# Kernel tuning notes

Hardware: AMD Instinct MI355X
Metric: run time of the kernel (lower is better)

## Reference

```python
import jax, jax.numpy as jnp
import numpy as np

INPUT_SIZE = 128
HIDDEN_SIZE = 256


def lstm_cell(x, h, c, w_ih, w_hh, b_ih, b_hh):
    # PyTorch LSTMCell gate order: i, f, g, o
    gates = x @ w_ih.T + b_ih + h @ w_hh.T + b_hh  # [B, 4H]
    i, f, g, o = jnp.split(gates, 4, axis=-1)
    c_new = jax.nn.sigmoid(f) * c + jax.nn.sigmoid(i) * jnp.tanh(g)
    h_new = jax.nn.sigmoid(o) * jnp.tanh(c_new)
    return h_new, c_new


def setup_inputs() -> dict:
    key = jax.random.key(0)
    ks = jax.random.split(key, 7)
    P, H = INPUT_SIZE, HIDDEN_SIZE
    s_ih = 1.0 / np.sqrt(H)
    inputs = jax.random.normal(ks[0], (8, 256, 64, P), dtype=jnp.float32)
    w_ih = jax.random.uniform(ks[1], (4 * H, P), jnp.float32, -s_ih, s_ih)
    w_hh = jax.random.uniform(ks[2], (4 * H, H), jnp.float32, -s_ih, s_ih)
    b_ih = jax.random.uniform(ks[3], (4 * H,), jnp.float32, -s_ih, s_ih)
    b_hh = jax.random.uniform(ks[4], (4 * H,), jnp.float32, -s_ih, s_ih)
    s_l = 1.0 / np.sqrt(H)
    w_lin = jax.random.uniform(ks[5], (P, H), jnp.float32, -s_l, s_l)
    b_lin = jax.random.uniform(ks[6], (P,), jnp.float32, -s_l, s_l)
    return {"inputs": inputs, "w_ih": w_ih, "w_hh": w_hh, "b_ih": b_ih,
            "b_hh": b_hh, "w_lin": w_lin, "b_lin": b_lin, "horizon": 32}


def reference(inputs, w_ih, w_hh, b_ih, b_hh, w_lin, b_lin, horizon):
    T, S, F, P = inputs.shape
    H = w_hh.shape[1]
    B = T * S  # tasks share weights, states are independent -> fuse batch
    x = inputs.reshape(B, F, P)
    h0 = jnp.zeros((B, H), inputs.dtype)
    c0 = jnp.zeros((B, H), inputs.dtype)

    def enc_step(carry, xt):
        h, c = carry
        h, c = lstm_cell(xt, h, c, w_ih, w_hh, b_ih, b_hh)
        return (h, c), None

    (h, c), _ = jax.lax.scan(enc_step, (h0, c0), jnp.swapaxes(x, 0, 1))
    pred = h @ w_lin.T + b_lin  # [B, P]

    def ar_step(carry, _):
        h, c, p = carry
        h, c = lstm_cell(p, h, c, w_ih, w_hh, b_ih, b_hh)
        p = h @ w_lin.T + b_lin
        return (h, c, p), p

    _, preds = jax.lax.scan(ar_step, (h, c, pred), None, length=horizon - 1)
    outs = jnp.concatenate([pred[None], preds], axis=0)  # [horizon, B, P]
    return jnp.moveaxis(outs, 0, 1).reshape(T, S, horizon, P)
```

## Files before the change

### kernel.cpp

```cpp
#include <hip/hip_runtime.h>
#include <cstdint>
#include <cstddef>

typedef short short8_t __attribute__((ext_vector_type(8)));
typedef float float4_t __attribute__((ext_vector_type(4)));

#define NRG 32

__device__ __align__(16) unsigned short g_W[1024 * 384];
__device__ __align__(16) unsigned short g_Weff[1024 * 256];
__device__ __align__(16) unsigned short g_Wlin[128 * 256];
__device__ float g_bias[1024];
__device__ float g_beff[1024];
__device__ float g_blin[128];
__device__ __align__(16) unsigned short g_hx[NRG][2][64][256];
__device__ int g_flag[NRG][4][8];

__device__ __forceinline__ unsigned short f2bf_rn(float f) {
    union { float f; unsigned int u; } v; v.f = f;
    unsigned int u = v.u;
    return (unsigned short)((u + 0x7FFFu + ((u >> 16) & 1u)) >> 16);
}
__device__ __forceinline__ float sigm(float x) { return 1.0f / (1.0f + __expf(-x)); }
__device__ __forceinline__ float tanh_fast(float x) { return 2.0f / (1.0f + __expf(-2.0f * x)) - 1.0f; }

__global__ void prep_kernel(const float* __restrict__ w_ih, const float* __restrict__ w_hh,
                            const float* __restrict__ b_ih, const float* __restrict__ b_hh,
                            const float* __restrict__ w_lin, const float* __restrict__ b_lin) {
    int idx = blockIdx.x * blockDim.x + threadIdx.x;
    int stride = gridDim.x * blockDim.x;
    for (int i = idx; i < 49152; i += stride) {
        int f = i >> 6, l = i & 63;
        int kt = f % 12, rest = f / 12;
        int s = rest & 3, wvv = (rest >> 2) & 3, g = rest >> 4;
        int n = g * 256 + wvv * 64 + s * 16 + (l & 15);
        int k0 = kt * 32 + (l >> 4) * 8;
        unsigned short* dst = g_W + f * 512 + l * 8;
#pragma unroll
        for (int j = 0; j < 8; ++j) {
            int k = k0 + j;
            float v = (k < 128) ? w_ih[n * 128 + k] : w_hh[n * 256 + (k - 128)];
            dst[j] = f2bf_rn(v);
        }
    }
    for (int i = idx; i < 4096; i += stride) {
        int f = i >> 6, l = i & 63;
        int kt = f & 7, wss = f >> 3;
        int s = wss & 1, wvv = wss >> 1;
        int n = wvv * 32 + s * 16 + (l & 15);
        int k0 = kt * 32 + (l >> 4) * 8;
        unsigned short* dst = g_Wlin + f * 512 + l * 8;
#pragma unroll
        for (int j = 0; j < 8; ++j)
            dst[j] = f2bf_rn(w_lin[n * 256 + k0 + j]);
    }
    for (int i = idx; i < 1024; i += stride) g_bias[i] = b_ih[i] + b_hh[i];
    for (int i = idx; i < 128; i += stride) g_blin[i] = b_lin[i];
    for (int i = idx; i < NRG * 32; i += stride) ((int*)g_flag)[i] = 0;
}

__global__ void prep2_kernel(const float* __restrict__ w_ih, const float* __restrict__ w_hh,
                             const float* __restrict__ w_lin, const float* __restrict__ b_ih,
                             const float* __restrict__ b_hh, const float* __restrict__ b_lin) {
    int i = blockIdx.x * 256 + threadIdx.x;
    {
        int e = i & 511, f = i >> 9;
        int l = e >> 3, j = e & 7;
        int kt2 = f & 7, rest = f >> 3;
        int s = rest & 3, w = (rest >> 2) & 3, g = rest >> 4;
        int n = g * 256 + w * 64 + s * 16 + (l & 15);
        int k = kt2 * 32 + (l >> 4) * 8 + j;
        float acc = w_hh[n * 256 + k];
#pragma unroll 4
        for (int p = 0; p < 128; ++p)
            acc += w_ih[n * 128 + p] * w_lin[p * 256 + k];
        g_Weff[f * 512 + e] = f2bf_rn(acc);
    }
    if (i < 1024) {
        float acc = b_ih[i] + b_hh[i];
        for (int p = 0; p < 128; ++p)
            acc += w_ih[i * 128 + p] * b_lin[p];
        g_beff[i] = acc;
    }
}

__global__ void __launch_bounds__(256, 1) lstm_persist(const float* __restrict__ inp,
                                                       float* __restrict__ out) {
    __shared__ __align__(16) unsigned short gw[96 * 512];
    __shared__ __align__(16) unsigned short wl_sh[8 * 512];
    __shared__ __align__(16) unsigned short tb[4][512];

    const int tid = threadIdx.x;
    const int wv = tid >> 6, l = tid & 63, l15 = l & 15, lg = l >> 4;
    const int c = blockIdx.x >> 5, rg = blockIdx.x & 31;

    for (int i = tid; i < 96 * 64; i += 256) {
        int lf = i >> 6, ch = i & 63;
        int kt = lf % 12, gs = lf / 12;
        int s2 = gs & 1, g = gs >> 1;
        int gf = ((g * 4 + (c >> 1)) * 4 + 2 * (c & 1) + s2) * 12 + kt;
        *(uint4*)&gw[lf * 512 + ch * 8] = *(const uint4*)&g_W[gf * 512 + ch * 8];
    }
    for (int i = tid; i < 8 * 64; i += 256) {
        int lf = i >> 6, ch = i & 63;
        *(uint4*)&wl_sh[lf * 512 + ch * 8] = *(const uint4*)&g_Wlin[(c * 8 + lf) * 512 + ch * 8];
    }
    float biasr[4][2], beffr[4][2];
#pragma unroll
    for (int g = 0; g < 4; ++g)
#pragma unroll
        for (int s2 = 0; s2 < 2; ++s2) {
            biasr[g][s2] = g_bias[g * 256 + c * 32 + s2 * 16 + l15];
            beffr[g][s2] = g_beff[g * 256 + c * 32 + s2 * 16 + l15];
        }
    const float blin_r = g_blin[c * 16 + l15];
    __syncthreads();

    short8_t ha[8], xa[4];
    short8_t zz = {0, 0, 0, 0, 0, 0, 0, 0};
#pragma unroll
    for (int i = 0; i < 8; ++i) ha[i] = zz;
#pragma unroll
    for (int i = 0; i < 4; ++i) xa[i] = zz;
    float c_st[2][4];
#pragma unroll
    for (int s2 = 0; s2 < 2; ++s2)
#pragma unroll
        for (int r = 0; r < 4; ++r) c_st[s2][r] = 0.0f;

    const float* xrow = inp + (size_t)(rg * 64 + wv * 16 + l15) * 8192 + lg * 8;
    float4_t xf[8];
#pragma unroll
    for (int kt = 0; kt < 4; ++kt) {
        xf[2 * kt]     = *(const float4_t*)(xrow + kt * 32);
        xf[2 * kt + 1] = *(const float4_t*)(xrow + kt * 32 + 4);
    }

    for (int t = 0; t <= 95; ++t) {
        if (t == 64) {
            __syncthreads();
            for (int i = tid; i < 64 * 64; i += 256) {
                int lf = i >> 6, ch = i & 63;
                int kt2 = lf & 7, gs = lf >> 3;
                int s2 = gs & 1, g = gs >> 1;
                int gf = ((g * 4 + (c >> 1)) * 4 + 2 * (c & 1) + s2) * 8 + kt2;
                *(uint4*)&gw[lf * 512 + ch * 8] = *(const uint4*)&g_Weff[gf * 512 + ch * 8];
            }
            __syncthreads();
        }

        float4_t acc[4][2];
        if (t < 95) {
#pragma unroll
            for (int g = 0; g < 4; ++g)
#pragma unroll
                for (int s2 = 0; s2 < 2; ++s2) {
                    float b = (t < 64) ? biasr[g][s2] : beffr[g][s2];
                    acc[g][s2] = (float4_t){b, b, b, b};
                }
        }

        if (t < 64) {
#pragma unroll
            for (int kt = 0; kt < 4; ++kt) {
                short8_t vv;
                vv[0] = (short)f2bf_rn(xf[2 * kt][0]); vv[1] = (short)f2bf_rn(xf[2 * kt][1]);
                vv[2] = (short)f2bf_rn(xf[2 * kt][2]); vv[3] = (short)f2bf_rn(xf[2 * kt][3]);
                vv[4] = (short)f2bf_rn(xf[2 * kt + 1][0]); vv[5] = (short)f2bf_rn(xf[2 * kt + 1][1]);
                vv[6] = (short)f2bf_rn(xf[2 * kt + 1][2]); vv[7] = (short)f2bf_rn(xf[2 * kt + 1][3]);
                xa[kt] = vv;
            }
            if (t <= 62) {
                const float* xp = xrow + (t + 1) * 128;
#pragma unroll
                for (int kt = 0; kt < 4; ++kt) {
                    xf[2 * kt]     = *(const float4_t*)(xp + kt * 32);
                    xf[2 * kt + 1] = *(const float4_t*)(xp + kt * 32 + 4);
                }
            }
#pragma unroll
            for (int kt = 0; kt < 4; ++kt)
#pragma unroll
                for (int g = 0; g < 4; ++g)
#pragma unroll
                    for (int s2 = 0; s2 < 2; ++s2) {
                        const short8_t wf = *(const short8_t*)&gw[((g * 2 + s2) * 12 + kt) * 512 + l * 8];
                        acc[g][s2] = __builtin_amdgcn_mfma_f32_16x16x32_bf16(xa[kt], wf, acc[g][s2], 0, 0, 0);
                    }
        }

        if (t > 0) {
            __builtin_amdgcn_sched_barrier(0);
            const int* fp = &g_flag[rg][wv][l & 7];
            int fv, guard = 0;
            do {
                asm volatile("global_load_dword %0, %1, off sc0 sc1\n\ts_waitcnt vmcnt(0)"
                             : "=v"(fv) : "v"(fp) : "memory");
            } while (!__all(fv >= t) && ++guard < (1 << 15));
            __builtin_amdgcn_sched_barrier(0);
            const char* hb = (const char*)&g_hx[rg][(t - 1) & 1][wv * 16 + l15][lg * 8];
#pragma unroll
            for (int kt = 0; kt < 8; ++kt)
                asm volatile("global_load_dwordx4 %0, %1, off sc0 sc1"
                             : "=v"(ha[kt]) : "v"(hb + kt * 64) : "memory");
            asm volatile("s_waitcnt vmcnt(0)" ::: "memory");
            __builtin_amdgcn_sched_barrier(0);
        }

        if (t < 95) {
            if (t > 0) {
                if (t < 64) {
#pragma unroll
                    for (int kt = 4; kt < 12; ++kt)
#pragma unroll
                        for (int g = 0; g < 4; ++g)
#pragma unroll
                            for (int s2 = 0; s2 < 2; ++s2) {
                                const short8_t wf = *(const short8_t*)&gw[((g * 2 + s2) * 12 + kt) * 512 + l * 8];
                                acc[g][s2] = __builtin_amdgcn_mfma_f32_16x16x32_bf16(ha[kt - 4], wf, acc[g][s2], 0, 0, 0);
                            }
                } else {
#pragma unroll
                    for (int kt = 0; kt < 8; ++kt)
#pragma unroll
                        for (int g = 0; g < 4; ++g)
#pragma unroll
                            for (int s2 = 0; s2 < 2; ++s2) {
                                const short8_t wf = *(const short8_t*)&gw[((g * 2 + s2) * 8 + kt) * 512 + l * 8];
                                acc[g][s2] = __builtin_amdgcn_mfma_f32_16x16x32_bf16(ha[kt], wf, acc[g][s2], 0, 0, 0);
                            }
                }
            }
            char* tbw = (char*)&tb[wv][0];
#pragma unroll
            for (int s2 = 0; s2 < 2; ++s2)
#pragma unroll
                for (int r = 0; r < 4; ++r) {
                    float ip = acc[0][s2][r], fpv = acc[1][s2][r];
                    float gp = acc[2][s2][r], op = acc[3][s2][r];
                    float cn = sigm(fpv) * c_st[s2][r] + sigm(ip) * tanh_fast(gp);
                    c_st[s2][r] = cn;
                    float hv = sigm(op) * tanh_fast(cn);
                    int m = lg * 4 + r;
                    int boff = (m * 64 + (s2 * 16 + l15) * 2) ^ (lg << 4);
                    *(unsigned short*)(tbw + boff) = f2bf_rn(hv);
                }
            int roff = (l15 * 64 + (lg << 4)) ^ ((l15 >> 2) << 4);
            short8_t hv8 = *(const short8_t*)(tbw + roff);
            char* dst = (char*)&g_hx[rg][t & 1][wv * 16 + l15][c * 32 + lg * 8];
            asm volatile("global_store_dwordx4 %0, %1, off sc0 sc1" :: "v"(dst), "v"(hv8) : "memory");
            asm volatile("s_waitcnt vmcnt(0)" ::: "memory");
            if (l == 0) {
                int* fw = &g_flag[rg][wv][c];
                int nv = t + 1;
                asm volatile("global_store_dword %0, %1, off sc0 sc1" :: "v"(fw), "v"(nv) : "memory");
            }
        }

        if (t >= 64) {
            float4_t pacc = {blin_r, blin_r, blin_r, blin_r};
#pragma unroll
            for (int kt = 0; kt < 8; ++kt) {
                const short8_t wf = *(const short8_t*)&wl_sh[kt * 512 + l * 8];
                pacc = __builtin_amdgcn_mfma_f32_16x16x32_bf16(ha[kt], wf, pacc, 0, 0, 0);
            }
            int ko = t - 64;
            float* orow = out + ((size_t)(rg * 64 + wv * 16 + lg * 4) * 32 + ko) * 128 + c * 16 + l15;
#pragma unroll
            for (int r = 0; r < 4; ++r)
                orow[(size_t)r * 32 * 128] = pacc[r];
        }
    }
}

extern "C" void kernel_launch(void* const* d_in, const int* in_sizes, int n_in,
                              void* d_out, int out_size, void* d_ws, size_t ws_size,
                              hipStream_t stream) {
    const float* inp   = (const float*)d_in[0];
    const float* w_ih  = (const float*)d_in[1];
    const float* w_hh  = (const float*)d_in[2];
    const float* b_ih  = (const float*)d_in[3];
    const float* b_hh  = (const float*)d_in[4];
    const float* w_lin = (const float*)d_in[5];
    const float* b_lin = (const float*)d_in[6];
    (void)in_sizes; (void)n_in; (void)d_ws; (void)ws_size; (void)out_size;

    prep_kernel<<<128, 256, 0, stream>>>(w_ih, w_hh, b_ih, b_hh, w_lin, b_lin);
    prep2_kernel<<<1024, 256, 0, stream>>>(w_ih, w_hh, w_lin, b_ih, b_hh, b_lin);
    lstm_persist<<<256, 256, 0, stream>>>(inp, (float*)d_out);
}
```

Baseline: 606.2 us.

## Interleave two row groups per block to hide cross-block sync latency

Each persistent block now handles two independent row groups (A and B) and alternates between them. While one group's compute runs, the flag poll and the hidden-state loads for the other group are already in flight, which is meant to hide the global-memory handoff between blocks on the recurrence. The grid is halved to 128 blocks, so half as many CUs are in use and each block does twice the MFMA work per step. The spin guard limit is also raised.

```diff
diff --git a/kernel.cpp b/kernel.cpp
--- a/kernel.cpp
+++ b/kernel.cpp
@@ -84,6 +84,124 @@
     }
 }
 
+#define WAITCNT0 do { asm volatile("s_waitcnt vmcnt(0)" ::: "memory"); \
+                      __builtin_amdgcn_sched_barrier(0); } while (0)
+
+#define POLL(RG, WANT) do { \
+    __builtin_amdgcn_sched_barrier(0); \
+    const int* fp_ = &g_flag[RG][wv][l & 7]; \
+    int fv_, guard_ = 0; \
+    do { \
+        asm volatile("global_load_dword %0, %1, off sc0 sc1\n\ts_waitcnt vmcnt(0)" \
+                     : "=v"(fv_) : "v"(fp_) : "memory"); \
+    } while (!__all(fv_ >= (WANT)) && ++guard_ < (1 << 18)); \
+    __builtin_amdgcn_sched_barrier(0); \
+} while (0)
+
+#define ISSUE_HA(HA, RG, PAR) do { \
+    const char* hb_ = (const char*)&g_hx[RG][PAR][wv * 16 + l15][lg * 8]; \
+    _Pragma("unroll") \
+    for (int kt_ = 0; kt_ < 8; ++kt_) \
+        asm volatile("global_load_dwordx4 %0, %1, off sc0 sc1" \
+                     : "=v"(HA[kt_]) : "v"(hb_ + kt_ * 64) : "memory"); \
+} while (0)
+
+#define ISSUE_XF(XF, XROW, TT) do { \
+    const char* xp_ = (const char*)((XROW) + (size_t)(TT) * 128); \
+    _Pragma("unroll") \
+    for (int q_ = 0; q_ < 8; ++q_) \
+        asm volatile("global_load_dwordx4 %0, %1, off" \
+                     : "=v"(XF[q_]) : "v"(xp_ + ((q_ >> 1) * 128 + (q_ & 1) * 16)) : "memory"); \
+} while (0)
+
+#define CONVERT_XA(XF) do { \
+    _Pragma("unroll") \
+    for (int kt_ = 0; kt_ < 4; ++kt_) { \
+        short8_t vv_; \
+        vv_[0] = (short)f2bf_rn(XF[2*kt_][0]); vv_[1] = (short)f2bf_rn(XF[2*kt_][1]); \
+        vv_[2] = (short)f2bf_rn(XF[2*kt_][2]); vv_[3] = (short)f2bf_rn(XF[2*kt_][3]); \
+        vv_[4] = (short)f2bf_rn(XF[2*kt_+1][0]); vv_[5] = (short)f2bf_rn(XF[2*kt_+1][1]); \
+        vv_[6] = (short)f2bf_rn(XF[2*kt_+1][2]); vv_[7] = (short)f2bf_rn(XF[2*kt_+1][3]); \
+        xa[kt_] = vv_; \
+    } \
+} while (0)
+
+#define XPART() do { \
+    _Pragma("unroll") \
+    for (int kt_ = 0; kt_ < 4; ++kt_) \
+        _Pragma("unroll") \
+        for (int g_ = 0; g_ < 4; ++g_) \
+            _Pragma("unroll") \
+            for (int s2_ = 0; s2_ < 2; ++s2_) { \
+                const short8_t wf_ = *(const short8_t*)&gw[((g_*2+s2_)*12+kt_)*512 + l*8]; \
+                acc[g_][s2_] = __builtin_amdgcn_mfma_f32_16x16x32_bf16(xa[kt_], wf_, acc[g_][s2_], 0, 0, 0); \
+            } \
+} while (0)
+
+#define HPART_ENC(HA) do { \
+    _Pragma("unroll") \
+    for (int kt_ = 4; kt_ < 12; ++kt_) \
+        _Pragma("unroll") \
+        for (int g_ = 0; g_ < 4; ++g_) \
+            _Pragma("unroll") \
+            for (int s2_ = 0; s2_ < 2; ++s2_) { \
+                const short8_t wf_ = *(const short8_t*)&gw[((g_*2+s2_)*12+kt_)*512 + l*8]; \
+                acc[g_][s2_] = __builtin_amdgcn_mfma_f32_16x16x32_bf16(HA[kt_-4], wf_, acc[g_][s2_], 0, 0, 0); \
+            } \
+} while (0)
+
+#define HPART_AR(HA) do { \
+    _Pragma("unroll") \
+    for (int kt_ = 0; kt_ < 8; ++kt_) \
+        _Pragma("unroll") \
+        for (int g_ = 0; g_ < 4; ++g_) \
+            _Pragma("unroll") \
+            for (int s2_ = 0; s2_ < 2; ++s2_) { \
+                const short8_t wf_ = *(const short8_t*)&gw[((g_*2+s2_)*8+kt_)*512 + l*8]; \
+                acc[g_][s2_] = __builtin_amdgcn_mfma_f32_16x16x32_bf16(HA[kt_], wf_, acc[g_][s2_], 0, 0, 0); \
+            } \
+} while (0)
+
+#define POINTWISE_STORE(RG, CST, PAR, FLAGVAL) do { \
+    char* tbw_ = (char*)&tb[wv][0]; \
+    _Pragma("unroll") \
+    for (int s2_ = 0; s2_ < 2; ++s2_) \
+        _Pragma("unroll") \
+        for (int r_ = 0; r_ < 4; ++r_) { \
+            float ip_ = acc[0][s2_][r_], fp2_ = acc[1][s2_][r_]; \
+            float gp_ = acc[2][s2_][r_], op_ = acc[3][s2_][r_]; \
+            float cn_ = sigm(fp2_) * CST[s2_][r_] + sigm(ip_) * tanh_fast(gp_); \
+            CST[s2_][r_] = cn_; \
+            float hv_ = sigm(op_) * tanh_fast(cn_); \
+            int m_ = lg * 4 + r_; \
+            int boff_ = (m_ * 64 + (s2_ * 16 + l15) * 2) ^ (lg << 4); \
+            *(unsigned short*)(tbw_ + boff_) = f2bf_rn(hv_); \
+        } \
+    int roff_ = (l15 * 64 + (lg << 4)) ^ ((l15 >> 2) << 4); \
+    short8_t hv8_ = *(const short8_t*)(tbw_ + roff_); \
+    char* dst_ = (char*)&g_hx[RG][PAR][wv * 16 + l15][c * 32 + lg * 8]; \
+    asm volatile("global_store_dwordx4 %0, %1, off sc0 sc1" :: "v"(dst_), "v"(hv8_) : "memory"); \
+    WAITCNT0; \
+    if (l == 0) { \
+        int* fw_ = &g_flag[RG][wv][c]; \
+        int nv_ = (FLAGVAL); \
+        asm volatile("global_store_dword %0, %1, off sc0 sc1" :: "v"(fw_), "v"(nv_) : "memory"); \
+    } \
+} while (0)
+
+#define PRED(HA, RG, KO) do { \
+    float4_t pacc_ = {blin_r, blin_r, blin_r, blin_r}; \
+    _Pragma("unroll") \
+    for (int kt_ = 0; kt_ < 8; ++kt_) { \
+        const short8_t wf_ = *(const short8_t*)&wl_sh[kt_ * 512 + l * 8]; \
+        pacc_ = __builtin_amdgcn_mfma_f32_16x16x32_bf16(HA[kt_], wf_, pacc_, 0, 0, 0); \
+    } \
+    float* orow_ = out + ((size_t)((RG) * 64 + wv * 16 + lg * 4) * 32 + (KO)) * 128 + c * 16 + l15; \
+    _Pragma("unroll") \
+    for (int r_ = 0; r_ < 4; ++r_) \
+        orow_[(size_t)r_ * 32 * 128] = pacc_[r_]; \
+} while (0)
+
 __global__ void __launch_bounds__(256, 1) lstm_persist(const float* __restrict__ inp,
                                                        float* __restrict__ out) {
     __shared__ __align__(16) unsigned short gw[96 * 512];
@@ -92,7 +210,8 @@
 
     const int tid = threadIdx.x;
     const int wv = tid >> 6, l = tid & 63, l15 = l & 15, lg = l >> 4;
-    const int c = blockIdx.x >> 5, rg = blockIdx.x & 31;
+    const int c = blockIdx.x >> 4, srg = blockIdx.x & 15;
+    const int rgA = 2 * srg, rgB = 2 * srg + 1;
 
     for (int i = tid; i < 96 * 64; i += 256) {
         int lf = i >> 6, ch = i & 63;
@@ -116,25 +235,18 @@
     const float blin_r = g_blin[c * 16 + l15];
     __syncthreads();
 
-    short8_t ha[8], xa[4];
-    short8_t zz = {0, 0, 0, 0, 0, 0, 0, 0};
-#pragma unroll
-    for (int i = 0; i < 8; ++i) ha[i] = zz;
-#pragma unroll
-    for (int i = 0; i < 4; ++i) xa[i] = zz;
-    float c_st[2][4];
+    short8_t haA[8], haB[8], xa[4];
+    float4_t xfA[8], xfB[8];
+    float cA[2][4], cB[2][4];
 #pragma unroll
     for (int s2 = 0; s2 < 2; ++s2)
 #pragma unroll
-        for (int r = 0; r < 4; ++r) c_st[s2][r] = 0.0f;
-
-    const float* xrow = inp + (size_t)(rg * 64 + wv * 16 + l15) * 8192 + lg * 8;
-    float4_t xf[8];
-#pragma unroll
-    for (int kt = 0; kt < 4; ++kt) {
-        xf[2 * kt]     = *(const float4_t*)(xrow + kt * 32);
-        xf[2 * kt + 1] = *(const float4_t*)(xrow + kt * 32 + 4);
-    }
+        for (int r = 0; r < 4; ++r) { cA[s2][r] = 0.0f; cB[s2][r] = 0.0f; }
+
+    const float* xrowA = inp + (size_t)(rgA * 64 + wv * 16 + l15) * 8192 + lg * 8;
+    const float* xrowB = inp + (size_t)(rgB * 64 + wv * 16 + l15) * 8192 + lg * 8;
+    ISSUE_XF(xfA, xrowA, 0);
+    ISSUE_XF(xfB, xrowB, 0);
 
     for (int t = 0; t <= 95; ++t) {
         if (t == 64) {
@@ -148,127 +260,53 @@
             }
             __syncthreads();
         }
-
-        float4_t acc[4][2];
+        const bool enc = (t < 64);
+
+        if (t > 0) {
+            POLL(rgB, t);
+            ISSUE_HA(haB, rgB, (t - 1) & 1);
+        } else {
+            WAITCNT0;
+        }
+
         if (t < 95) {
+            float4_t acc[4][2];
 #pragma unroll
             for (int g = 0; g < 4; ++g)
 #pragma unroll
                 for (int s2 = 0; s2 < 2; ++s2) {
-                    float b = (t < 64) ? biasr[g][s2] : beffr[g][s2];
+                    float b = enc ? biasr[g][s2] : beffr[g][s2];
                     acc[g][s2] = (float4_t){b, b, b, b};
                 }
-        }
-
-        if (t < 64) {
-#pragma unroll
-            for (int kt = 0; kt < 4; ++kt) {
-                short8_t vv;
-                vv[0] = (short)f2bf_rn(xf[2 * kt][0]); vv[1] = (short)f2bf_rn(xf[2 * kt][1]);
-                vv[2] = (short)f2bf_rn(xf[2 * kt][2]); vv[3] = (short)f2bf_rn(xf[2 * kt][3]);
-                vv[4] = (short)f2bf_rn(xf[2 * kt + 1][0]); vv[5] = (short)f2bf_rn(xf[2 * kt + 1][1]);
-                vv[6] = (short)f2bf_rn(xf[2 * kt + 1][2]); vv[7] = (short)f2bf_rn(xf[2 * kt + 1][3]);
-                xa[kt] = vv;
-            }
-            if (t <= 62) {
-                const float* xp = xrow + (t + 1) * 128;
-#pragma unroll
-                for (int kt = 0; kt < 4; ++kt) {
-                    xf[2 * kt]     = *(const float4_t*)(xp + kt * 32);
-                    xf[2 * kt + 1] = *(const float4_t*)(xp + kt * 32 + 4);
+            if (enc) { CONVERT_XA(xfA); XPART(); }
+            if (t > 0) { if (enc) HPART_ENC(haA); else HPART_AR(haA); }
+            POINTWISE_STORE(rgA, cA, t & 1, t + 1);
+        }
+        if (t >= 64) PRED(haA, rgA, t - 64);
+
+        if (t < 95) {
+            POLL(rgA, t + 1);
+            ISSUE_HA(haA, rgA, t & 1);
+            if (t <= 62) ISSUE_XF(xfA, xrowA, t + 1);
+        }
+
+        if (t < 95) {
+            float4_t acc[4][2];
+#pragma unroll
+            for (int g = 0; g < 4; ++g)
+#pragma unroll
+                for (int s2 = 0; s2 < 2; ++s2) {
+                    float b = enc ? biasr[g][s2] : beffr[g][s2];
+                    acc[g][s2] = (float4_t){b, b, b, b};
                 }
-            }
-#pragma unroll
-            for (int kt = 0; kt < 4; ++kt)
-#pragma unroll
-                for (int g = 0; g < 4; ++g)
-#pragma unroll
-                    for (int s2 = 0; s2 < 2; ++s2) {
-                        const short8_t wf = *(const short8_t*)&gw[((g * 2 + s2) * 12 + kt) * 512 + l * 8];
-                        acc[g][s2] = __builtin_amdgcn_mfma_f32_16x16x32_bf16(xa[kt], wf, acc[g][s2], 0, 0, 0);
-                    }
-        }
-
-        if (t > 0) {
-            __builtin_amdgcn_sched_barrier(0);
-            const int* fp = &g_flag[rg][wv][l & 7];
-            int fv, guard = 0;
-            do {
-                asm volatile("global_load_dword %0, %1, off sc0 sc1\n\ts_waitcnt vmcnt(0)"
-                             : "=v"(fv) : "v"(fp) : "memory");
-            } while (!__all(fv >= t) && ++guard < (1 << 15));
-            __builtin_amdgcn_sched_barrier(0);
-            const char* hb = (const char*)&g_hx[rg][(t - 1) & 1][wv * 16 + l15][lg * 8];
-#pragma unroll
-            for (int kt = 0; kt < 8; ++kt)
-                asm volatile("global_load_dwordx4 %0, %1, off sc0 sc1"
-                             : "=v"(ha[kt]) : "v"(hb + kt * 64) : "memory");
-            asm volatile("s_waitcnt vmcnt(0)" ::: "memory");
-            __builtin_amdgcn_sched_barrier(0);
-        }
-
-        if (t < 95) {
-            if (t > 0) {
-                if (t < 64) {
-#pragma unroll
-                    for (int kt = 4; kt < 12; ++kt)
-#pragma unroll
-                        for (int g = 0; g < 4; ++g)
-#pragma unroll
-                            for (int s2 = 0; s2 < 2; ++s2) {
-                                const short8_t wf = *(const short8_t*)&gw[((g * 2 + s2) * 12 + kt) * 512 + l * 8];
-                                acc[g][s2] = __builtin_amdgcn_mfma_f32_16x16x32_bf16(ha[kt - 4], wf, acc[g][s2], 0, 0, 0);
-                            }
-                } else {
-#pragma unroll
-                    for (int kt = 0; kt < 8; ++kt)
-#pragma unroll
-                        for (int g = 0; g < 4; ++g)
-#pragma unroll
-                            for (int s2 = 0; s2 < 2; ++s2) {
-                                const short8_t wf = *(const short8_t*)&gw[((g * 2 + s2) * 8 + kt) * 512 + l * 8];
-                                acc[g][s2] = __builtin_amdgcn_mfma_f32_16x16x32_bf16(ha[kt], wf, acc[g][s2], 0, 0, 0);
-                            }
-                }
-            }
-            char* tbw = (char*)&tb[wv][0];
-#pragma unroll
-            for (int s2 = 0; s2 < 2; ++s2)
-#pragma unroll
-                for (int r = 0; r < 4; ++r) {
-                    float ip = acc[0][s2][r], fpv = acc[1][s2][r];
-                    float gp = acc[2][s2][r], op = acc[3][s2][r];
-                    float cn = sigm(fpv) * c_st[s2][r] + sigm(ip) * tanh_fast(gp);
-                    c_st[s2][r] = cn;
-                    float hv = sigm(op) * tanh_fast(cn);
-                    int m = lg * 4 + r;
-                    int boff = (m * 64 + (s2 * 16 + l15) * 2) ^ (lg << 4);
-                    *(unsigned short*)(tbw + boff) = f2bf_rn(hv);
-                }
-            int roff = (l15 * 64 + (lg << 4)) ^ ((l15 >> 2) << 4);
-            short8_t hv8 = *(const short8_t*)(tbw + roff);
-            char* dst = (char*)&g_hx[rg][t & 1][wv * 16 + l15][c * 32 + lg * 8];
-            asm volatile("global_store_dwordx4 %0, %1, off sc0 sc1" :: "v"(dst), "v"(hv8) : "memory");
-            asm volatile("s_waitcnt vmcnt(0)" ::: "memory");
-            if (l == 0) {
-                int* fw = &g_flag[rg][wv][c];
-                int nv = t + 1;
-                asm volatile("global_store_dword %0, %1, off sc0 sc1" :: "v"(fw), "v"(nv) : "memory");
-            }
-        }
-
+            if (enc) { CONVERT_XA(xfB); XPART(); }
+            if (t > 0) { if (enc) HPART_ENC(haB); else HPART_AR(haB); }
+            POINTWISE_STORE(rgB, cB, t & 1, t + 1);
+            if (t <= 62) ISSUE_XF(xfB, xrowB, t + 1);
+        }
         if (t >= 64) {
-            float4_t pacc = {blin_r, blin_r, blin_r, blin_r};
-#pragma unroll
-            for (int kt = 0; kt < 8; ++kt) {
-                const short8_t wf = *(const short8_t*)&wl_sh[kt * 512 + l * 8];
-                pacc = __builtin_amdgcn_mfma_f32_16x16x32_bf16(ha[kt], wf, pacc, 0, 0, 0);
-            }
-            int ko = t - 64;
-            float* orow = out + ((size_t)(rg * 64 + wv * 16 + lg * 4) * 32 + ko) * 128 + c * 16 + l15;
-#pragma unroll
-            for (int r = 0; r < 4; ++r)
-                orow[(size_t)r * 32 * 128] = pacc[r];
+            if (t == 95) WAITCNT0;
+            PRED(haB, rgB, t - 64);
         }
     }
 }
@@ -287,5 +325,5 @@
 
     prep_kernel<<<128, 256, 0, stream>>>(w_ih, w_hh, b_ih, b_hh, w_lin, b_lin);
     prep2_kernel<<<1024, 256, 0, stream>>>(w_ih, w_hh, w_lin, b_ih, b_hh, b_lin);
-    lstm_persist<<<256, 256, 0, stream>>>(inp, (float*)d_out);
-}
+    lstm_persist<<<128, 256, 0, stream>>>(inp, (float*)d_out);
+}
```

Result: slower. 1.411 ms (+132.8%).

## Keep each 16-row batch tile in one block, exchanging h through LDS

Applied to the files above, without the earlier changes.

Restructures the persistent LSTM kernel so that one 1024-thread block owns 16 batch rows and all 1024 gate columns. Each of its 16 waves holds its weight slice in registers. Before, 8 blocks split the columns of each row group and exchanged h through global memory using flag spin-waits. Now h is shared through double-buffered swizzled LDS with __syncthreads, removing global round-trips and polling latency per timestep. The trade-off is heavy register pressure (48 short8 weight fragments per lane), and only 128 blocks are launched, which may underuse CUs and risks spills.

```diff
diff --git a/kernel.cpp b/kernel.cpp
--- a/kernel.cpp
+++ b/kernel.cpp
@@ -4,8 +4,6 @@
 
 typedef short short8_t __attribute__((ext_vector_type(8)));
 typedef float float4_t __attribute__((ext_vector_type(4)));
-
-#define NRG 32
 
 __device__ __align__(16) unsigned short g_W[1024 * 384];
 __device__ __align__(16) unsigned short g_Weff[1024 * 256];
@@ -13,8 +11,6 @@
 __device__ float g_bias[1024];
 __device__ float g_beff[1024];
 __device__ float g_blin[128];
-__device__ __align__(16) unsigned short g_hx[NRG][2][64][256];
-__device__ int g_flag[NRG][4][8];
 
 __device__ __forceinline__ unsigned short f2bf_rn(float f) {
     union { float f; unsigned int u; } v; v.f = f;
@@ -56,7 +52,6 @@
     }
     for (int i = idx; i < 1024; i += stride) g_bias[i] = b_ih[i] + b_hh[i];
     for (int i = idx; i < 128; i += stride) g_blin[i] = b_lin[i];
-    for (int i = idx; i < NRG * 32; i += stride) ((int*)g_flag)[i] = 0;
 }
 
 __global__ void prep2_kernel(const float* __restrict__ w_ih, const float* __restrict__ w_hh,
@@ -84,83 +79,104 @@
     }
 }
 
-__global__ void __launch_bounds__(256, 1) lstm_persist(const float* __restrict__ inp,
-                                                       float* __restrict__ out) {
-    __shared__ __align__(16) unsigned short gw[96 * 512];
-    __shared__ __align__(16) unsigned short wl_sh[8 * 512];
-    __shared__ __align__(16) unsigned short tb[4][512];
+__global__ void __launch_bounds__(1024, 1) lstm_persist(const float* __restrict__ inp,
+                                                        float* __restrict__ out) {
+    __shared__ __align__(16) unsigned short h_lds[2][16 * 256];
 
     const int tid = threadIdx.x;
-    const int wv = tid >> 6, l = tid & 63, l15 = l & 15, lg = l >> 4;
-    const int c = blockIdx.x >> 5, rg = blockIdx.x & 31;
-
-    for (int i = tid; i < 96 * 64; i += 256) {
-        int lf = i >> 6, ch = i & 63;
-        int kt = lf % 12, gs = lf / 12;
-        int s2 = gs & 1, g = gs >> 1;
-        int gf = ((g * 4 + (c >> 1)) * 4 + 2 * (c & 1) + s2) * 12 + kt;
-        *(uint4*)&gw[lf * 512 + ch * 8] = *(const uint4*)&g_W[gf * 512 + ch * 8];
-    }
-    for (int i = tid; i < 8 * 64; i += 256) {
-        int lf = i >> 6, ch = i & 63;
-        *(uint4*)&wl_sh[lf * 512 + ch * 8] = *(const uint4*)&g_Wlin[(c * 8 + lf) * 512 + ch * 8];
-    }
-    float biasr[4][2], beffr[4][2];
+    const int w = tid >> 6, l = tid & 63, l15 = l & 15, lg = l >> 4;
+    const int blk = blockIdx.x;
+
+    short8_t wreg[48];
 #pragma unroll
     for (int g = 0; g < 4; ++g)
 #pragma unroll
-        for (int s2 = 0; s2 < 2; ++s2) {
-            biasr[g][s2] = g_bias[g * 256 + c * 32 + s2 * 16 + l15];
-            beffr[g][s2] = g_beff[g * 256 + c * 32 + s2 * 16 + l15];
-        }
-    const float blin_r = g_blin[c * 16 + l15];
-    __syncthreads();
-
+        for (int kt = 0; kt < 12; ++kt) {
+            int f = g * 192 + (w >> 2) * 48 + (w & 3) * 12 + kt;
+            wreg[g * 12 + kt] = *(const short8_t*)&g_W[f * 512 + l * 8];
+        }
+    short8_t wlreg[8];
+    if (w < 8) {
+#pragma unroll
+        for (int kt = 0; kt < 8; ++kt)
+            wlreg[kt] = *(const short8_t*)&g_Wlin[(w * 8 + kt) * 512 + l * 8];
+    }
+    float biasr[4], beffr[4];
+#pragma unroll
+    for (int g = 0; g < 4; ++g) {
+        biasr[g] = g_bias[g * 256 + w * 16 + l15];
+        beffr[g] = g_beff[g * 256 + w * 16 + l15];
+    }
+    const float blin_r = (w < 8) ? g_blin[w * 16 + l15] : 0.0f;
+
+    float c_st[4] = {0.0f, 0.0f, 0.0f, 0.0f};
     short8_t ha[8], xa[4];
-    short8_t zz = {0, 0, 0, 0, 0, 0, 0, 0};
-#pragma unroll
-    for (int i = 0; i < 8; ++i) ha[i] = zz;
-#pragma unroll
-    for (int i = 0; i < 4; ++i) xa[i] = zz;
-    float c_st[2][4];
-#pragma unroll
-    for (int s2 = 0; s2 < 2; ++s2)
-#pragma unroll
-        for (int r = 0; r < 4; ++r) c_st[s2][r] = 0.0f;
-
-    const float* xrow = inp + (size_t)(rg * 64 + wv * 16 + l15) * 8192 + lg * 8;
     float4_t xf[8];
+
+    const float* xrow = inp + (size_t)(blk * 16 + l15) * 8192 + lg * 8;
 #pragma unroll
     for (int kt = 0; kt < 4; ++kt) {
         xf[2 * kt]     = *(const float4_t*)(xrow + kt * 32);
         xf[2 * kt + 1] = *(const float4_t*)(xrow + kt * 32 + 4);
     }
-
-    for (int t = 0; t <= 95; ++t) {
-        if (t == 64) {
-            __syncthreads();
-            for (int i = tid; i < 64 * 64; i += 256) {
-                int lf = i >> 6, ch = i & 63;
-                int kt2 = lf & 7, gs = lf >> 3;
-                int s2 = gs & 1, g = gs >> 1;
-                int gf = ((g * 4 + (c >> 1)) * 4 + 2 * (c & 1) + s2) * 8 + kt2;
-                *(uint4*)&gw[lf * 512 + ch * 8] = *(const uint4*)&g_Weff[gf * 512 + ch * 8];
-            }
-            __syncthreads();
-        }
-
-        float4_t acc[4][2];
-        if (t < 95) {
+#pragma unroll
+    for (int kt = 0; kt < 4; ++kt) {
+        short8_t vv;
+        vv[0] = (short)f2bf_rn(xf[2 * kt][0]); vv[1] = (short)f2bf_rn(xf[2 * kt][1]);
+        vv[2] = (short)f2bf_rn(xf[2 * kt][2]); vv[3] = (short)f2bf_rn(xf[2 * kt][3]);
+        vv[4] = (short)f2bf_rn(xf[2 * kt + 1][0]); vv[5] = (short)f2bf_rn(xf[2 * kt + 1][1]);
+        vv[6] = (short)f2bf_rn(xf[2 * kt + 1][2]); vv[7] = (short)f2bf_rn(xf[2 * kt + 1][3]);
+        xa[kt] = vv;
+    }
+
+    for (int t = 0; t < 64; ++t) {
+        if (t < 63) {
+            const float* xp = xrow + (t + 1) * 128;
+#pragma unroll
+            for (int kt = 0; kt < 4; ++kt) {
+                xf[2 * kt]     = *(const float4_t*)(xp + kt * 32);
+                xf[2 * kt + 1] = *(const float4_t*)(xp + kt * 32 + 4);
+            }
+        }
+
+        float4_t acc[4];
+#pragma unroll
+        for (int g = 0; g < 4; ++g)
+            acc[g] = (float4_t){biasr[g], biasr[g], biasr[g], biasr[g]};
+
+#pragma unroll
+        for (int kt = 0; kt < 4; ++kt)
 #pragma unroll
             for (int g = 0; g < 4; ++g)
-#pragma unroll
-                for (int s2 = 0; s2 < 2; ++s2) {
-                    float b = (t < 64) ? biasr[g][s2] : beffr[g][s2];
-                    acc[g][s2] = (float4_t){b, b, b, b};
-                }
-        }
-
-        if (t < 64) {
+                acc[g] = __builtin_amdgcn_mfma_f32_16x16x32_bf16(xa[kt], wreg[g * 12 + kt], acc[g], 0, 0, 0);
+
+        if (t > 0) {
+            const char* hb = (const char*)&h_lds[(t - 1) & 1][0];
+#pragma unroll
+            for (int kt = 0; kt < 8; ++kt) {
+                int off = (l15 * 512 + kt * 64 + lg * 16) ^ ((l15 & 7) << 4);
+                ha[kt] = *(const short8_t*)(hb + off);
+            }
+#pragma unroll
+            for (int kt = 0; kt < 8; ++kt)
+#pragma unroll
+                for (int g = 0; g < 4; ++g)
+                    acc[g] = __builtin_amdgcn_mfma_f32_16x16x32_bf16(ha[kt], wreg[g * 12 + 4 + kt], acc[g], 0, 0, 0);
+        }
+
+        char* hwb = (char*)&h_lds[t & 1][0];
+#pragma unroll
+        for (int r = 0; r < 4; ++r) {
+            float ip = acc[0][r], fp = acc[1][r], gp = acc[2][r], op = acc[3][r];
+            float cn = sigm(fp) * c_st[r] + sigm(ip) * tanh_fast(gp);
+            c_st[r] = cn;
+            float hv = sigm(op) * tanh_fast(cn);
+            int row = lg * 4 + r, col = w * 16 + l15;
+            int off = (row * 512 + col * 2) ^ ((row & 7) << 4);
+            *(unsigned short*)(hwb + off) = f2bf_rn(hv);
+        }
+
+        if (t < 63) {
 #pragma unroll
             for (int kt = 0; kt < 4; ++kt) {
                 short8_t vv;
@@ -170,106 +186,63 @@
                 vv[6] = (short)f2bf_rn(xf[2 * kt + 1][2]); vv[7] = (short)f2bf_rn(xf[2 * kt + 1][3]);
                 xa[kt] = vv;
             }
-            if (t <= 62) {
-                const float* xp = xrow + (t + 1) * 128;
-#pragma unroll
-                for (int kt = 0; kt < 4; ++kt) {
-                    xf[2 * kt]     = *(const float4_t*)(xp + kt * 32);
-                    xf[2 * kt + 1] = *(const float4_t*)(xp + kt * 32 + 4);
-                }
-            }
-#pragma unroll
-            for (int kt = 0; kt < 4; ++kt)
+        }
+        __syncthreads();
+    }
+
+#pragma unroll
+    for (int g = 0; g < 4; ++g)
+#pragma unroll
+        for (int kt = 0; kt < 8; ++kt) {
+            int f = g * 128 + (w >> 2) * 32 + (w & 3) * 8 + kt;
+            wreg[g * 8 + kt] = *(const short8_t*)&g_Weff[f * 512 + l * 8];
+        }
+
+    for (int t = 64; t <= 95; ++t) {
+        const char* hb = (const char*)&h_lds[(t - 1) & 1][0];
+#pragma unroll
+        for (int kt = 0; kt < 8; ++kt) {
+            int off = (l15 * 512 + kt * 64 + lg * 16) ^ ((l15 & 7) << 4);
+            ha[kt] = *(const short8_t*)(hb + off);
+        }
+
+        if (t < 95) {
+            float4_t acc[4];
+#pragma unroll
+            for (int g = 0; g < 4; ++g)
+                acc[g] = (float4_t){beffr[g], beffr[g], beffr[g], beffr[g]};
+#pragma unroll
+            for (int kt = 0; kt < 8; ++kt)
 #pragma unroll
                 for (int g = 0; g < 4; ++g)
-#pragma unroll
-                    for (int s2 = 0; s2 < 2; ++s2) {
-                        const short8_t wf = *(const short8_t*)&gw[((g * 2 + s2) * 12 + kt) * 512 + l * 8];
-                        acc[g][s2] = __builtin_amdgcn_mfma_f32_16x16x32_bf16(xa[kt], wf, acc[g][s2], 0, 0, 0);
-                    }
-        }
-
-        if (t > 0) {
-            __builtin_amdgcn_sched_barrier(0);
-            const int* fp = &g_flag[rg][wv][l & 7];
-            int fv, guard = 0;
-            do {
-                asm volatile("global_load_dword %0, %1, off sc0 sc1\n\ts_waitcnt vmcnt(0)"
-                             : "=v"(fv) : "v"(fp) : "memory");
-            } while (!__all(fv >= t) && ++guard < (1 << 15));
-            __builtin_amdgcn_sched_barrier(0);
-            const char* hb = (const char*)&g_hx[rg][(t - 1) & 1][wv * 16 + l15][lg * 8];
+                    acc[g] = __builtin_amdgcn_mfma_f32_16x16x32_bf16(ha[kt], wreg[g * 8 + kt], acc[g], 0, 0, 0);
+
+            char* hwb = (char*)&h_lds[t & 1][0];
+#pragma unroll
+            for (int r = 0; r < 4; ++r) {
+                float ip = acc[0][r], fp = acc[1][r], gp = acc[2][r], op = acc[3][r];
+                float cn = sigm(fp) * c_st[r] + sigm(ip) * tanh_fast(gp);
+                c_st[r] = cn;
+                float hv = sigm(op) * tanh_fast(cn);
+                int row = lg * 4 + r, col = w * 16 + l15;
+                int off = (row * 512 + col * 2) ^ ((row & 7) << 4);
+                *(unsigned short*)(hwb + off) = f2bf_rn(hv);
+            }
+        }
+
+        if (w < 8) {
+            float4_t pacc = {blin_r, blin_r, blin_r, blin_r};
 #pragma unroll
             for (int kt = 0; kt < 8; ++kt)
-                asm volatile("global_load_dwordx4 %0, %1, off sc0 sc1"
-                             : "=v"(ha[kt]) : "v"(hb + kt * 64) : "memory");
-            asm volatile("s_waitcnt vmcnt(0)" ::: "memory");
-            __builtin_amdgcn_sched_barrier(0);
-        }
-
-        if (t < 95) {
-            if (t > 0) {
-                if (t < 64) {
-#pragma unroll
-                    for (int kt = 4; kt < 12; ++kt)
-#pragma unroll
-                        for (int g = 0; g < 4; ++g)
-#pragma unroll
-                            for (int s2 = 0; s2 < 2; ++s2) {
-                                const short8_t wf = *(const short8_t*)&gw[((g * 2 + s2) * 12 + kt) * 512 + l * 8];
-                                acc[g][s2] = __builtin_amdgcn_mfma_f32_16x16x32_bf16(ha[kt - 4], wf, acc[g][s2], 0, 0, 0);
-                            }
-                } else {
-#pragma unroll
-                    for (int kt = 0; kt < 8; ++kt)
-#pragma unroll
-                        for (int g = 0; g < 4; ++g)
-#pragma unroll
-                            for (int s2 = 0; s2 < 2; ++s2) {
-                                const short8_t wf = *(const short8_t*)&gw[((g * 2 + s2) * 8 + kt) * 512 + l * 8];
-                                acc[g][s2] = __builtin_amdgcn_mfma_f32_16x16x32_bf16(ha[kt], wf, acc[g][s2], 0, 0, 0);
-                            }
-                }
-            }
-            char* tbw = (char*)&tb[wv][0];
-#pragma unroll
-            for (int s2 = 0; s2 < 2; ++s2)
-#pragma unroll
-                for (int r = 0; r < 4; ++r) {
-                    float ip = acc[0][s2][r], fpv = acc[1][s2][r];
-                    float gp = acc[2][s2][r], op = acc[3][s2][r];
-                    float cn = sigm(fpv) * c_st[s2][r] + sigm(ip) * tanh_fast(gp);
-                    c_st[s2][r] = cn;
-                    float hv = sigm(op) * tanh_fast(cn);
-                    int m = lg * 4 + r;
-                    int boff = (m * 64 + (s2 * 16 + l15) * 2) ^ (lg << 4);
-                    *(unsigned short*)(tbw + boff) = f2bf_rn(hv);
-                }
-            int roff = (l15 * 64 + (lg << 4)) ^ ((l15 >> 2) << 4);
-            short8_t hv8 = *(const short8_t*)(tbw + roff);
-            char* dst = (char*)&g_hx[rg][t & 1][wv * 16 + l15][c * 32 + lg * 8];
-            asm volatile("global_store_dwordx4 %0, %1, off sc0 sc1" :: "v"(dst), "v"(hv8) : "memory");
-            asm volatile("s_waitcnt vmcnt(0)" ::: "memory");
-            if (l == 0) {
-                int* fw = &g_flag[rg][wv][c];
-                int nv = t + 1;
-                asm volatile("global_store_dword %0, %1, off sc0 sc1" :: "v"(fw), "v"(nv) : "memory");
-            }
-        }
-
-        if (t >= 64) {
-            float4_t pacc = {blin_r, blin_r, blin_r, blin_r};
-#pragma unroll
-            for (int kt = 0; kt < 8; ++kt) {
-                const short8_t wf = *(const short8_t*)&wl_sh[kt * 512 + l * 8];
-                pacc = __builtin_amdgcn_mfma_f32_16x16x32_bf16(ha[kt], wf, pacc, 0, 0, 0);
-            }
+                pacc = __builtin_amdgcn_mfma_f32_16x16x32_bf16(ha[kt], wlreg[kt], pacc, 0, 0, 0);
             int ko = t - 64;
-            float* orow = out + ((size_t)(rg * 64 + wv * 16 + lg * 4) * 32 + ko) * 128 + c * 16 + l15;
+            float* orow = out + ((size_t)(blk * 16 + lg * 4) * 32 + ko) * 128 + w * 16 + l15;
 #pragma unroll
             for (int r = 0; r < 4; ++r)
                 orow[(size_t)r * 32 * 128] = pacc[r];
         }
+
+        if (t < 95) __syncthreads();
     }
 }
 
@@ -287,5 +260,5 @@
 
     prep_kernel<<<128, 256, 0, stream>>>(w_ih, w_hh, b_ih, b_hh, w_lin, b_lin);
     prep2_kernel<<<1024, 256, 0, stream>>>(w_ih, w_hh, w_lin, b_ih, b_hh, b_lin);
-    lstm_persist<<<256, 256, 0, stream>>>(inp, (float*)d_out);
-}
+    lstm_persist<<<128, 1024, 0, stream>>>(inp, (float*)d_out);
+}
```

After: 1.838 ms. 3.03x slower.
